# Performance work log

Hardware: AMD Instinct MI355X
Metric: run time of the kernel (lower is better)

Reference implementation:

```python
import jax, jax.numpy as jnp
import numpy as np

B, T, D_MODEL, H = 2, 2048, 1024, 16
D_HEAD = D_MODEL // H


def setup_inputs() -> dict:
    key = jax.random.key(0)
    k1, k2, k3 = jax.random.split(key, 3)
    x = jax.random.normal(k1, (B, T, D_MODEL), dtype=jnp.float32)
    # Linear weights stored as (in, out); scale like torch default init roughly
    W_qkv = jax.random.normal(k2, (D_MODEL, 3 * D_MODEL), dtype=jnp.float32) / np.sqrt(D_MODEL)
    W_o = jax.random.normal(k3, (D_MODEL, D_MODEL), dtype=jnp.float32) / np.sqrt(D_MODEL)
    return {"x": x, "W_qkv": W_qkv, "W_o": W_o}


def reference(x, W_qkv, W_o):
    Bx, Tx, C = x.shape
    qkv = x @ W_qkv                                   # (B,T,3C)
    qkv = qkv.reshape(Bx, Tx, 3, H, D_HEAD)
    q = qkv[:, :, 0].transpose(0, 2, 1, 3)            # (B,H,T,D)
    k = qkv[:, :, 1].transpose(0, 2, 1, 3)
    v = qkv[:, :, 2].transpose(0, 2, 1, 3)
    scale = 1.0 / np.sqrt(D_HEAD).astype(np.float32)
    att = jnp.einsum('bhqd,bhkd->bhqk', q, k) * scale  # (B,H,T,T)
    causal = jnp.tril(jnp.ones((Tx, Tx), dtype=bool))
    att = jnp.where(causal[None, None], att, jnp.float32(-jnp.inf))
    w = jax.nn.softmax(att, axis=-1)
    out = jnp.einsum('bhqk,bhkd->bhqd', w, v)          # (B,H,T,D)
    out = out.transpose(0, 2, 1, 3).reshape(Bx, Tx, C)
    return out @ W_o
```

## Files before the change

kernel.cpp:

```cpp
#include <hip/hip_runtime.h>

typedef unsigned short u16;
typedef unsigned int u32;
typedef __bf16 bf16x8 __attribute__((ext_vector_type(8)));
typedef float f32x4 __attribute__((ext_vector_type(4)));

#define DEV __device__ __forceinline__

constexpr int BB = 2;
constexpr int TT = 2048;
constexpr int CD = 1024;
constexpr int HH = 16;
constexpr int DH = 64;
constexpr int BT = BB * TT;

DEV u16 f2bf(float f) {
    u32 u = __builtin_bit_cast(u32, f);
    u32 r = u + 0x7FFFu + ((u >> 16) & 1u);
    return (u16)(r >> 16);
}

DEV f32x4 mfma16(bf16x8 a, bf16x8 b, f32x4 c) {
    return __builtin_amdgcn_mfma_f32_16x16x32_bf16(a, b, c, 0, 0, 0);
}

DEV void gld_lds16(u16* lds, const u16* g) {
    __builtin_amdgcn_global_load_lds(
        (const __attribute__((address_space(1))) unsigned int*)g,
        (__attribute__((address_space(3))) unsigned int*)lds, 16, 0, 0);
}

__global__ __launch_bounds__(256)
void convert_f32_bf16(const float* __restrict__ in, u16* __restrict__ out, int n) {
    const int i = (blockIdx.x * 256 + threadIdx.x) * 8;
    if (i >= n) return;
    float4 a = *(const float4*)&in[i];
    float4 b = *(const float4*)&in[i + 4];
    u16 t[8];
    t[0] = f2bf(a.x); t[1] = f2bf(a.y); t[2] = f2bf(a.z); t[3] = f2bf(a.w);
    t[4] = f2bf(b.x); t[5] = f2bf(b.y); t[6] = f2bf(b.z); t[7] = f2bf(b.w);
    *(uint4*)&out[i] = *(const uint4*)t;
}

__global__ __launch_bounds__(256)
void transpose_f32_bf16(const float* __restrict__ in, u16* __restrict__ out,
                        int rows, int cols) {
    __shared__ u16 tile[32][33];
    const int c0 = blockIdx.x * 32, r0 = blockIdx.y * 32;
    const int tx = threadIdx.x, ty = threadIdx.y;
    #pragma unroll
    for (int i = ty; i < 32; i += 8)
        tile[i][tx] = f2bf(in[(r0 + i) * cols + (c0 + tx)]);
    __syncthreads();
    #pragma unroll
    for (int i = ty; i < 32; i += 8)
        out[(c0 + i) * rows + (r0 + tx)] = tile[tx][i];
}

template <int EPI>
__global__ __launch_bounds__(256)
void gemm_bt(const u16* __restrict__ A, const u16* __restrict__ Bt,
             u16* __restrict__ out0, u16* __restrict__ out1,
             u16* __restrict__ out2, float* __restrict__ outf,
             int M, int N, int K) {
    constexpr int BM = 128, BN = 128, BK = 32, AST = 32;
    __shared__ alignas(16) u16 As[BM * AST];
    __shared__ alignas(16) u16 Bs[BN * AST];

    const int tid  = threadIdx.x;
    const int wave = tid >> 6, lane = tid & 63;
    const int quad = lane >> 4, l16 = lane & 15;
    const int wm = (wave & 1) * 64, wn = (wave >> 1) * 64;
    const int m0 = blockIdx.y * BM, n0 = blockIdx.x * BN;

    const int srow = wave * 32 + (lane >> 2);
    const int scol = (lane & 3) * 8;
    const u16* ga0 = A  + (size_t)(m0 + srow) * K + scol;
    const u16* ga1 = ga0 + (size_t)16 * K;
    const u16* gb0 = Bt + (size_t)(n0 + srow) * K + scol;
    const u16* gb1 = gb0 + (size_t)16 * K;
    u16* la0 = As + wave * 1024;
    u16* la1 = As + wave * 1024 + 512;
    u16* lb0 = Bs + wave * 1024;
    u16* lb1 = Bs + wave * 1024 + 512;

    f32x4 acc[4][4] = {};

    for (int k0 = 0; k0 < K; k0 += BK) {
        gld_lds16(la0, ga0 + k0);
        gld_lds16(la1, ga1 + k0);
        gld_lds16(lb0, gb0 + k0);
        gld_lds16(lb1, gb1 + k0);
        __syncthreads();

        bf16x8 fa[4], fb[4];
        #pragma unroll
        for (int mt = 0; mt < 4; ++mt)
            fa[mt] = *(const bf16x8*)&As[(wm + mt * 16 + l16) * AST + quad * 8];
        #pragma unroll
        for (int nt = 0; nt < 4; ++nt)
            fb[nt] = *(const bf16x8*)&Bs[(wn + nt * 16 + l16) * AST + quad * 8];
        #pragma unroll
        for (int mt = 0; mt < 4; ++mt)
            #pragma unroll
            for (int nt = 0; nt < 4; ++nt)
                acc[mt][nt] = mfma16(fa[mt], fb[nt], acc[mt][nt]);
        __syncthreads();
    }

    #pragma unroll
    for (int mt = 0; mt < 4; ++mt) {
        #pragma unroll
        for (int nt = 0; nt < 4; ++nt) {
            #pragma unroll
            for (int reg = 0; reg < 4; ++reg) {
                const int r = m0 + wm + mt * 16 + quad * 4 + reg;
                const int c = n0 + wn + nt * 16 + l16;
                if (EPI == 0) {
                    outf[(size_t)r * N + c] = acc[mt][nt][reg];
                } else {
                    const int which = c >> 10;
                    const int cc = c & 1023;
                    const int h = cc >> 6, d = cc & 63;
                    const int b = r >> 11, t = r & 2047;
                    const int bh = b * HH + h;
                    if (which == 0) {
                        out0[((size_t)bh * TT + t) * DH + d] =
                            f2bf(acc[mt][nt][reg] * 0.125f);
                    } else if (which == 1) {
                        out1[((size_t)bh * TT + t) * DH + d] = f2bf(acc[mt][nt][reg]);
                    } else {
                        out2[((size_t)bh * DH + d) * TT + t] = f2bf(acc[mt][nt][reg]);
                    }
                }
            }
        }
    }
}

constexpr int KST = 72;

DEV void attn_step(const u16* __restrict__ Ksb, const u16* __restrict__ Vsb,
                   const bf16x8* fq, f32x4* Oacc,
                   float& m_i, float& l_i, bool diag,
                   int wave, int quad, int l16) {
    f32x4 st[4];
    #pragma unroll
    for (int nt = 0; nt < 4; ++nt) {
        bf16x8 fk0 = *(const bf16x8*)&Ksb[(nt * 16 + l16) * KST + quad * 8];
        bf16x8 fk1 = *(const bf16x8*)&Ksb[(nt * 16 + l16) * KST + 32 + quad * 8];
        f32x4 t = {};
        t = mfma16(fk0, fq[0], t);
        t = mfma16(fk1, fq[1], t);
        st[nt] = t;
    }

    if (diag) {
        const int qg = wave * 16 + l16;
        #pragma unroll
        for (int nt = 0; nt < 4; ++nt)
            #pragma unroll
            for (int reg = 0; reg < 4; ++reg) {
                const int kg = nt * 16 + quad * 4 + reg;
                st[nt][reg] = (kg <= qg) ? st[nt][reg] : -INFINITY;
            }
    }

    float vmax = st[0][0];
    #pragma unroll
    for (int nt = 0; nt < 4; ++nt)
        #pragma unroll
        for (int reg = 0; reg < 4; ++reg)
            vmax = fmaxf(vmax, st[nt][reg]);
    vmax = fmaxf(vmax, __shfl_xor(vmax, 16, 64));
    vmax = fmaxf(vmax, __shfl_xor(vmax, 32, 64));

    const float mnew = fmaxf(m_i, vmax);
    const float alpha = __expf(m_i - mnew);
    m_i = mnew;

    float vsum = 0.f;
    #pragma unroll
    for (int nt = 0; nt < 4; ++nt)
        #pragma unroll
        for (int reg = 0; reg < 4; ++reg) {
            const float p = __expf(st[nt][reg] - mnew);
            st[nt][reg] = p;
            vsum += p;
        }
    vsum += __shfl_xor(vsum, 16, 64);
    vsum += __shfl_xor(vsum, 32, 64);
    l_i = l_i * alpha + vsum;

    #pragma unroll
    for (int dt = 0; dt < 4; ++dt)
        #pragma unroll
        for (int reg = 0; reg < 4; ++reg)
            Oacc[dt][reg] *= alpha;

    bf16x8 pb[4];
    #pragma unroll
    for (int nt = 0; nt < 4; ++nt) {
        u16 pa[8];
        #pragma unroll
        for (int reg = 0; reg < 4; ++reg) pa[reg] = f2bf(st[nt][reg]);
        pa[4] = pa[5] = pa[6] = pa[7] = 0;
        pb[nt] = *(const bf16x8*)pa;
    }

    #pragma unroll
    for (int nt = 0; nt < 4; ++nt) {
        #pragma unroll
        for (int dt = 0; dt < 4; ++dt) {
            u16 va[8];
            *(uint2*)va = *(const uint2*)&Vsb[(dt * 16 + l16) * KST + nt * 16 + quad * 4];
            va[4] = va[5] = va[6] = va[7] = 0;
            bf16x8 fv = *(const bf16x8*)va;
            Oacc[dt] = mfma16(fv, pb[nt], Oacc[dt]);
        }
    }
}

__global__ __launch_bounds__(256)
void attn_kernel(const u16* __restrict__ Q, const u16* __restrict__ Kb,
                 const u16* __restrict__ Vt, u16* __restrict__ O) {
    __shared__ alignas(16) u16 Ks[2][64 * KST];
    __shared__ alignas(16) u16 Vs[2][64 * KST];

    const int p = blockIdx.x;
    const int bh = blockIdx.y;
    const int qtA = 31 - p;
    const int qtB = p;
    const int jmax = qtA;

    const int tid = threadIdx.x;
    const int wave = tid >> 6, lane = tid & 63;
    const int quad = lane >> 4, l16 = lane & 15;

    const u16* Qh = Q  + (size_t)bh * TT * DH;
    const u16* Kh = Kb + (size_t)bh * TT * DH;
    const u16* Vh = Vt + (size_t)bh * DH * TT;

    const int rowA = qtA * 64 + wave * 16;
    const int rowB = qtB * 64 + wave * 16;

    bf16x8 fqA[2], fqB[2];
    fqA[0] = *(const bf16x8*)&Qh[(rowA + l16) * DH + quad * 8];
    fqA[1] = *(const bf16x8*)&Qh[(rowA + l16) * DH + 32 + quad * 8];
    fqB[0] = *(const bf16x8*)&Qh[(rowB + l16) * DH + quad * 8];
    fqB[1] = *(const bf16x8*)&Qh[(rowB + l16) * DH + 32 + quad * 8];

    f32x4 OA[4] = {}, OB[4] = {};
    float mA = -INFINITY, lA = 0.f, mB = -INFINITY, lB = 0.f;

    const int trow = tid >> 3, tcol = (tid & 7) * 8;
    uint4 kr0, kr1, vr0, vr1;

    auto load_chunk = [&](int j) {
        const u16* ks = Kh + (size_t)j * 64 * DH;
        kr0 = *(const uint4*)&ks[trow * DH + tcol];
        kr1 = *(const uint4*)&ks[(trow + 32) * DH + tcol];
        const u16* vs = Vh + (size_t)j * 64;
        vr0 = *(const uint4*)&vs[(size_t)trow * TT + tcol];
        vr1 = *(const uint4*)&vs[(size_t)(trow + 32) * TT + tcol];
    };
    auto write_chunk = [&](int buf) {
        *(uint4*)&Ks[buf][trow * KST + tcol]        = kr0;
        *(uint4*)&Ks[buf][(trow + 32) * KST + tcol] = kr1;
        *(uint4*)&Vs[buf][trow * KST + tcol]        = vr0;
        *(uint4*)&Vs[buf][(trow + 32) * KST + tcol] = vr1;
    };

    load_chunk(0);
    write_chunk(0);

    for (int j = 0; j <= jmax; ++j) {
        const int cur = j & 1;
        __syncthreads();
        if (j < jmax) load_chunk(j + 1);
        attn_step(Ks[cur], Vs[cur], fqA, OA, mA, lA, (j == qtA),
                  wave, quad, l16);
        if (j <= qtB)
            attn_step(Ks[cur], Vs[cur], fqB, OB, mB, lB, (j == qtB),
                      wave, quad, l16);
        if (j < jmax) write_chunk(cur ^ 1);
    }

    const int b = bh >> 4, h = bh & 15;
    const float rA = 1.f / lA, rB = 1.f / lB;
    #pragma unroll
    for (int dt = 0; dt < 4; ++dt) {
        u16 oa[4], ob[4];
        #pragma unroll
        for (int reg = 0; reg < 4; ++reg) {
            oa[reg] = f2bf(OA[dt][reg] * rA);
            ob[reg] = f2bf(OB[dt][reg] * rB);
        }
        *(uint2*)&O[((size_t)(b * TT + rowA + l16)) * CD + h * DH + dt * 16 + quad * 4] =
            *(const uint2*)oa;
        *(uint2*)&O[((size_t)(b * TT + rowB + l16)) * CD + h * DH + dt * 16 + quad * 4] =
            *(const uint2*)ob;
    }
}

extern "C" void kernel_launch(void* const* d_in, const int* in_sizes, int n_in,
                              void* d_out, int out_size, void* d_ws, size_t ws_size,
                              hipStream_t stream) {
    (void)in_sizes; (void)n_in; (void)out_size; (void)ws_size;
    const float* x    = (const float*)d_in[0];
    const float* Wqkv = (const float*)d_in[1];
    const float* Wo   = (const float*)d_in[2];
    float* out = (float*)d_out;

    char* ws = (char*)d_ws;
    u16* xb    = (u16*)(ws + 0);
    u16* WqkvT = (u16*)(ws + (8u  << 20));
    u16* WoT   = (u16*)(ws + (14u << 20));
    u16* Qb    = (u16*)(ws + (16u << 20));
    u16* Kb    = (u16*)(ws + (24u << 20));
    u16* Vt    = (u16*)(ws + (32u << 20));
    u16* attn  = (u16*)(ws + (40u << 20));

    convert_f32_bf16<<<BT * CD / (256 * 8), 256, 0, stream>>>(x, xb, BT * CD);
    transpose_f32_bf16<<<dim3(3072 / 32, 1024 / 32), dim3(32, 8), 0, stream>>>(
        Wqkv, WqkvT, 1024, 3072);
    transpose_f32_bf16<<<dim3(1024 / 32, 1024 / 32), dim3(32, 8), 0, stream>>>(
        Wo, WoT, 1024, 1024);

    gemm_bt<1><<<dim3(3072 / 128, BT / 128), 256, 0, stream>>>(
        xb, WqkvT, Qb, Kb, Vt, nullptr, BT, 3072, CD);

    attn_kernel<<<dim3(16, BB * HH), 256, 0, stream>>>(Qb, Kb, Vt, attn);

    gemm_bt<0><<<dim3(CD / 128, BT / 128), 256, 0, stream>>>(
        attn, WoT, nullptr, nullptr, nullptr, out, BT, CD, CD);
}
```

Measured before the change: 216.9 us.

## Fuse prep kernels, use full-K PV MFMAs, exp2 softmax, narrower output GEMM tile

Merges the x conversion and both weight transposes into a single prep launch. The attention kernel now permutes V as it is written to LDS so each PV MFMA uses all eight bf16 lanes instead of half-zero fragments. K/V fragments are loaded once per chunk and shared by both query tiles, and the softmax uses exp2 with log2(e) folded into the Q scale. The output projection uses BN=64 tiles to launch more blocks. Risks include higher register pressure from holding fragments (launch bounds now request 2 blocks/CU) and the correctness of the V permutation.

```diff
diff --git a/kernel.cpp b/kernel.cpp
--- a/kernel.cpp
+++ b/kernel.cpp
@@ -14,6 +14,8 @@
 constexpr int DH = 64;
 constexpr int BT = BB * TT;
 
+#define QSCALE 0.18033688011112042f
+
 DEV u16 f2bf(float f) {
     u32 u = __builtin_bit_cast(u32, f);
     u32 r = u + 0x7FFFu + ((u >> 16) & 1u);
@@ -31,23 +33,27 @@
 }
 
 __global__ __launch_bounds__(256)
-void convert_f32_bf16(const float* __restrict__ in, u16* __restrict__ out, int n) {
-    const int i = (blockIdx.x * 256 + threadIdx.x) * 8;
-    if (i >= n) return;
-    float4 a = *(const float4*)&in[i];
-    float4 b = *(const float4*)&in[i + 4];
-    u16 t[8];
-    t[0] = f2bf(a.x); t[1] = f2bf(a.y); t[2] = f2bf(a.z); t[3] = f2bf(a.w);
-    t[4] = f2bf(b.x); t[5] = f2bf(b.y); t[6] = f2bf(b.z); t[7] = f2bf(b.w);
-    *(uint4*)&out[i] = *(const uint4*)t;
-}
-
-__global__ __launch_bounds__(256)
-void transpose_f32_bf16(const float* __restrict__ in, u16* __restrict__ out,
-                        int rows, int cols) {
+void prep_kernel(const float* __restrict__ x, u16* __restrict__ xb,
+                 const float* __restrict__ Wqkv, u16* __restrict__ WqkvT,
+                 const float* __restrict__ Wo, u16* __restrict__ WoT) {
+    const int tid = threadIdx.x;
+    int blk = blockIdx.x;
+    if (blk < 2048) {
+        const int i = (blk * 256 + tid) * 8;
+        float4 a = *(const float4*)&x[i];
+        float4 b = *(const float4*)&x[i + 4];
+        u16 t[8];
+        t[0] = f2bf(a.x); t[1] = f2bf(a.y); t[2] = f2bf(a.z); t[3] = f2bf(a.w);
+        t[4] = f2bf(b.x); t[5] = f2bf(b.y); t[6] = f2bf(b.z); t[7] = f2bf(b.w);
+        *(uint4*)&xb[i] = *(const uint4*)t;
+        return;
+    }
     __shared__ u16 tile[32][33];
-    const int c0 = blockIdx.x * 32, r0 = blockIdx.y * 32;
-    const int tx = threadIdx.x, ty = threadIdx.y;
+    const float* in; u16* out; int rows, cols, bx, by;
+    if (blk < 5120) { blk -= 2048; in = Wqkv; out = WqkvT; rows = 1024; cols = 3072; bx = blk % 96; by = blk / 96; }
+    else            { blk -= 5120; in = Wo;   out = WoT;   rows = 1024; cols = 1024; bx = blk % 32; by = blk / 32; }
+    const int c0 = bx * 32, r0 = by * 32;
+    const int tx = tid & 31, ty = tid >> 5;
     #pragma unroll
     for (int i = ty; i < 32; i += 8)
         tile[i][tx] = f2bf(in[(r0 + i) * cols + (c0 + tx)]);
@@ -57,53 +63,55 @@
         out[(c0 + i) * rows + (r0 + tx)] = tile[tx][i];
 }
 
-template <int EPI>
+template <int EPI, int BN>
 __global__ __launch_bounds__(256)
 void gemm_bt(const u16* __restrict__ A, const u16* __restrict__ Bt,
              u16* __restrict__ out0, u16* __restrict__ out1,
              u16* __restrict__ out2, float* __restrict__ outf,
              int M, int N, int K) {
-    constexpr int BM = 128, BN = 128, BK = 32, AST = 32;
+    constexpr int BM = 128, BK = 32, AST = 32;
+    constexpr int NT = BN / 32;
     __shared__ alignas(16) u16 As[BM * AST];
     __shared__ alignas(16) u16 Bs[BN * AST];
 
     const int tid  = threadIdx.x;
     const int wave = tid >> 6, lane = tid & 63;
     const int quad = lane >> 4, l16 = lane & 15;
-    const int wm = (wave & 1) * 64, wn = (wave >> 1) * 64;
+    const int wm = (wave & 1) * 64, wn = (wave >> 1) * (BN / 2);
     const int m0 = blockIdx.y * BM, n0 = blockIdx.x * BN;
 
-    const int srow = wave * 32 + (lane >> 2);
-    const int scol = (lane & 3) * 8;
-    const u16* ga0 = A  + (size_t)(m0 + srow) * K + scol;
+    const int srowA = wave * 32 + (lane >> 2);
+    const int srowB = wave * (BN / 4) + (lane >> 2);
+    const int scol  = (lane & 3) * 8;
+    const u16* ga0 = A  + (size_t)(m0 + srowA) * K + scol;
     const u16* ga1 = ga0 + (size_t)16 * K;
-    const u16* gb0 = Bt + (size_t)(n0 + srow) * K + scol;
+    const u16* gb0 = Bt + (size_t)(n0 + srowB) * K + scol;
     const u16* gb1 = gb0 + (size_t)16 * K;
     u16* la0 = As + wave * 1024;
     u16* la1 = As + wave * 1024 + 512;
-    u16* lb0 = Bs + wave * 1024;
-    u16* lb1 = Bs + wave * 1024 + 512;
-
-    f32x4 acc[4][4] = {};
+    u16* lb0 = Bs + wave * (BN * 8);
+    u16* lb1 = Bs + wave * (BN * 8) + 512;
+
+    f32x4 acc[4][NT] = {};
 
     for (int k0 = 0; k0 < K; k0 += BK) {
         gld_lds16(la0, ga0 + k0);
         gld_lds16(la1, ga1 + k0);
         gld_lds16(lb0, gb0 + k0);
-        gld_lds16(lb1, gb1 + k0);
+        if constexpr (BN == 128) gld_lds16(lb1, gb1 + k0);
         __syncthreads();
 
-        bf16x8 fa[4], fb[4];
+        bf16x8 fa[4], fb[NT];
         #pragma unroll
         for (int mt = 0; mt < 4; ++mt)
             fa[mt] = *(const bf16x8*)&As[(wm + mt * 16 + l16) * AST + quad * 8];
         #pragma unroll
-        for (int nt = 0; nt < 4; ++nt)
+        for (int nt = 0; nt < NT; ++nt)
             fb[nt] = *(const bf16x8*)&Bs[(wn + nt * 16 + l16) * AST + quad * 8];
         #pragma unroll
         for (int mt = 0; mt < 4; ++mt)
             #pragma unroll
-            for (int nt = 0; nt < 4; ++nt)
+            for (int nt = 0; nt < NT; ++nt)
                 acc[mt][nt] = mfma16(fa[mt], fb[nt], acc[mt][nt]);
         __syncthreads();
     }
@@ -111,7 +119,7 @@
     #pragma unroll
     for (int mt = 0; mt < 4; ++mt) {
         #pragma unroll
-        for (int nt = 0; nt < 4; ++nt) {
+        for (int nt = 0; nt < NT; ++nt) {
             #pragma unroll
             for (int reg = 0; reg < 4; ++reg) {
                 const int r = m0 + wm + mt * 16 + quad * 4 + reg;
@@ -126,7 +134,7 @@
                     const int bh = b * HH + h;
                     if (which == 0) {
                         out0[((size_t)bh * TT + t) * DH + d] =
-                            f2bf(acc[mt][nt][reg] * 0.125f);
+                            f2bf(acc[mt][nt][reg] * QSCALE);
                     } else if (which == 1) {
                         out1[((size_t)bh * TT + t) * DH + d] = f2bf(acc[mt][nt][reg]);
                     } else {
@@ -140,18 +148,16 @@
 
 constexpr int KST = 72;
 
-DEV void attn_step(const u16* __restrict__ Ksb, const u16* __restrict__ Vsb,
+DEV void attn_step(const bf16x8 fk[4][2], const bf16x8 fv[2][4],
                    const bf16x8* fq, f32x4* Oacc,
                    float& m_i, float& l_i, bool diag,
                    int wave, int quad, int l16) {
     f32x4 st[4];
     #pragma unroll
     for (int nt = 0; nt < 4; ++nt) {
-        bf16x8 fk0 = *(const bf16x8*)&Ksb[(nt * 16 + l16) * KST + quad * 8];
-        bf16x8 fk1 = *(const bf16x8*)&Ksb[(nt * 16 + l16) * KST + 32 + quad * 8];
         f32x4 t = {};
-        t = mfma16(fk0, fq[0], t);
-        t = mfma16(fk1, fq[1], t);
+        t = mfma16(fk[nt][0], fq[0], t);
+        t = mfma16(fk[nt][1], fq[1], t);
         st[nt] = t;
     }
 
@@ -176,7 +182,7 @@
     vmax = fmaxf(vmax, __shfl_xor(vmax, 32, 64));
 
     const float mnew = fmaxf(m_i, vmax);
-    const float alpha = __expf(m_i - mnew);
+    const float alpha = __builtin_amdgcn_exp2f(m_i - mnew);
     m_i = mnew;
 
     float vsum = 0.f;
@@ -184,7 +190,7 @@
     for (int nt = 0; nt < 4; ++nt)
         #pragma unroll
         for (int reg = 0; reg < 4; ++reg) {
-            const float p = __expf(st[nt][reg] - mnew);
+            const float p = __builtin_amdgcn_exp2f(st[nt][reg] - mnew);
             st[nt][reg] = p;
             vsum += p;
         }
@@ -198,30 +204,22 @@
         for (int reg = 0; reg < 4; ++reg)
             Oacc[dt][reg] *= alpha;
 
-    bf16x8 pb[4];
-    #pragma unroll
-    for (int nt = 0; nt < 4; ++nt) {
+    #pragma unroll
+    for (int pair = 0; pair < 2; ++pair) {
         u16 pa[8];
         #pragma unroll
-        for (int reg = 0; reg < 4; ++reg) pa[reg] = f2bf(st[nt][reg]);
-        pa[4] = pa[5] = pa[6] = pa[7] = 0;
-        pb[nt] = *(const bf16x8*)pa;
-    }
-
-    #pragma unroll
-    for (int nt = 0; nt < 4; ++nt) {
-        #pragma unroll
-        for (int dt = 0; dt < 4; ++dt) {
-            u16 va[8];
-            *(uint2*)va = *(const uint2*)&Vsb[(dt * 16 + l16) * KST + nt * 16 + quad * 4];
-            va[4] = va[5] = va[6] = va[7] = 0;
-            bf16x8 fv = *(const bf16x8*)va;
-            Oacc[dt] = mfma16(fv, pb[nt], Oacc[dt]);
-        }
-    }
-}
-
-__global__ __launch_bounds__(256)
+        for (int j = 0; j < 4; ++j) {
+            pa[j]     = f2bf(st[2 * pair][j]);
+            pa[4 + j] = f2bf(st[2 * pair + 1][j]);
+        }
+        const bf16x8 pb = *(const bf16x8*)pa;
+        #pragma unroll
+        for (int dt = 0; dt < 4; ++dt)
+            Oacc[dt] = mfma16(fv[pair][dt], pb, Oacc[dt]);
+    }
+}
+
+__global__ __launch_bounds__(256, 2)
 void attn_kernel(const u16* __restrict__ Q, const u16* __restrict__ Kb,
                  const u16* __restrict__ Vt, u16* __restrict__ O) {
     __shared__ alignas(16) u16 Ks[2][64 * KST];
@@ -253,7 +251,10 @@
     f32x4 OA[4] = {}, OB[4] = {};
     float mA = -INFINITY, lA = 0.f, mB = -INFINITY, lB = 0.f;
 
-    const int trow = tid >> 3, tcol = (tid & 7) * 8;
+    const int trow = tid >> 3;
+    const int ic   = tid & 7;
+    const int tcol = ic * 8;
+    const int vc1 = 32 * (ic >> 2) + 16 * (ic & 1) + 4 * ((ic & 3) >> 1);
     uint4 kr0, kr1, vr0, vr1;
 
     auto load_chunk = [&](int j) {
@@ -267,8 +268,10 @@
     auto write_chunk = [&](int buf) {
         *(uint4*)&Ks[buf][trow * KST + tcol]        = kr0;
         *(uint4*)&Ks[buf][(trow + 32) * KST + tcol] = kr1;
-        *(uint4*)&Vs[buf][trow * KST + tcol]        = vr0;
-        *(uint4*)&Vs[buf][(trow + 32) * KST + tcol] = vr1;
+        *(uint2*)&Vs[buf][trow * KST + vc1]            = *(const uint2*)&vr0;
+        *(uint2*)&Vs[buf][trow * KST + vc1 + 8]        = *((const uint2*)&vr0 + 1);
+        *(uint2*)&Vs[buf][(trow + 32) * KST + vc1]     = *(const uint2*)&vr1;
+        *(uint2*)&Vs[buf][(trow + 32) * KST + vc1 + 8] = *((const uint2*)&vr1 + 1);
     };
 
     load_chunk(0);
@@ -278,11 +281,23 @@
         const int cur = j & 1;
         __syncthreads();
         if (j < jmax) load_chunk(j + 1);
-        attn_step(Ks[cur], Vs[cur], fqA, OA, mA, lA, (j == qtA),
-                  wave, quad, l16);
+
+        bf16x8 fk[4][2], fv[2][4];
+        #pragma unroll
+        for (int nt = 0; nt < 4; ++nt) {
+            fk[nt][0] = *(const bf16x8*)&Ks[cur][(nt * 16 + l16) * KST + quad * 8];
+            fk[nt][1] = *(const bf16x8*)&Ks[cur][(nt * 16 + l16) * KST + 32 + quad * 8];
+        }
+        #pragma unroll
+        for (int pair = 0; pair < 2; ++pair)
+            #pragma unroll
+            for (int dt = 0; dt < 4; ++dt)
+                fv[pair][dt] = *(const bf16x8*)
+                    &Vs[cur][(dt * 16 + l16) * KST + pair * 32 + quad * 8];
+
+        attn_step(fk, fv, fqA, OA, mA, lA, (j == qtA), wave, quad, l16);
         if (j <= qtB)
-            attn_step(Ks[cur], Vs[cur], fqB, OB, mB, lB, (j == qtB),
-                      wave, quad, l16);
+            attn_step(fk, fv, fqB, OB, mB, lB, (j == qtB), wave, quad, l16);
         if (j < jmax) write_chunk(cur ^ 1);
     }
 
@@ -321,17 +336,13 @@
     u16* Vt    = (u16*)(ws + (32u << 20));
     u16* attn  = (u16*)(ws + (40u << 20));
 
-    convert_f32_bf16<<<BT * CD / (256 * 8), 256, 0, stream>>>(x, xb, BT * CD);
-    transpose_f32_bf16<<<dim3(3072 / 32, 1024 / 32), dim3(32, 8), 0, stream>>>(
-        Wqkv, WqkvT, 1024, 3072);
-    transpose_f32_bf16<<<dim3(1024 / 32, 1024 / 32), dim3(32, 8), 0, stream>>>(
-        Wo, WoT, 1024, 1024);
-
-    gemm_bt<1><<<dim3(3072 / 128, BT / 128), 256, 0, stream>>>(
+    prep_kernel<<<6144, 256, 0, stream>>>(x, xb, Wqkv, WqkvT, Wo, WoT);
+
+    gemm_bt<1, 128><<<dim3(3072 / 128, BT / 128), 256, 0, stream>>>(
         xb, WqkvT, Qb, Kb, Vt, nullptr, BT, 3072, CD);
 
     attn_kernel<<<dim3(16, BB * HH), 256, 0, stream>>>(Qb, Kb, Vt, attn);
 
-    gemm_bt<0><<<dim3(CD / 128, BT / 128), 256, 0, stream>>>(
+    gemm_bt<0, 64><<<dim3(CD / 64, BT / 128), 256, 0, stream>>>(
         attn, WoT, nullptr, nullptr, nullptr, out, BT, CD, CD);
 }
```

New measurement: 190.7 us. 1.14x faster.
